# Kernel optimization log

Hardware: AMD Instinct MI355X
Metric: run time of the kernel (lower is better)

The kernel has to match this reference:

```python
import jax, jax.numpy as jnp
import numpy as np

EMB = 1024
HEADS = 16
HEAD_SZ = EMB // HEADS
EPS = 1e-5


def _layernorm(x, g, b):
    mu = jnp.mean(x, axis=-1, keepdims=True)
    var = jnp.mean(jnp.square(x - mu), axis=-1, keepdims=True)
    return (x - mu) * jax.lax.rsqrt(var + EPS) * g + b


def setup_inputs() -> dict:
    key = jax.random.key(0)
    ks = jax.random.split(key, 12)
    s_in = 1.0 / np.sqrt(EMB)
    s_h = 1.0 / np.sqrt(4 * EMB)
    return {
        "x": jax.random.normal(ks[0], (4, 1024, EMB), jnp.float32),
        # per-head Q/K/V projections stacked: [H, EMB, HEAD_SZ], no bias
        "wq": jax.random.normal(ks[1], (HEADS, EMB, HEAD_SZ), jnp.float32) * s_in,
        "wk": jax.random.normal(ks[2], (HEADS, EMB, HEAD_SZ), jnp.float32) * s_in,
        "wv": jax.random.normal(ks[3], (HEADS, EMB, HEAD_SZ), jnp.float32) * s_in,
        "w_proj": jax.random.normal(ks[4], (EMB, EMB), jnp.float32) * s_in,
        "b_proj": jnp.zeros((EMB,), jnp.float32),
        "w1": jax.random.normal(ks[5], (EMB, 4 * EMB), jnp.float32) * s_in,
        "b1": jnp.zeros((4 * EMB,), jnp.float32),
        "w2": jax.random.normal(ks[6], (4 * EMB, EMB), jnp.float32) * s_h,
        "b2": jnp.zeros((EMB,), jnp.float32),
        "g1": jnp.ones((EMB,), jnp.float32),
        "be1": jnp.zeros((EMB,), jnp.float32),
        "g2": jnp.ones((EMB,), jnp.float32),
        "be2": jnp.zeros((EMB,), jnp.float32),
    }


def reference(x, wq, wk, wv, w_proj, b_proj, w1, b1, w2, b2, g1, be1, g2, be2):
    B, T, C = x.shape
    # --- self-attention (pre-norm) ---
    h = _layernorm(x, g1, be1)
    q = jnp.einsum("btc,hcd->bhtd", h, wq)
    k = jnp.einsum("btc,hcd->bhtd", h, wk)
    v = jnp.einsum("btc,hcd->bhtd", h, wv)
    scale = 1.0 / jnp.sqrt(jnp.asarray(HEAD_SZ, x.dtype))
    scores = jnp.einsum("bhtd,bhsd->bhts", q, k) * scale  # non-causal: SDPA called with no mask
    attn = jax.nn.softmax(scores, axis=-1)
    o = jnp.einsum("bhts,bhsd->bhtd", attn, v)
    o = o.transpose(0, 2, 1, 3).reshape(B, T, C)  # concat heads (same order as torch.cat)
    sa_out = o @ w_proj + b_proj
    x = x + sa_out
    # --- feed-forward; note ln2 applied twice, faithful to source ---
    t = _layernorm(x, g2, be2)
    t = _layernorm(t, g2, be2)
    ff = jax.nn.relu(t @ w1 + b1) @ w2 + b2
    return x + ff
```

## Files before the change

### kernel.cpp

```cpp
#include <hip/hip_runtime.h>
#include <hip/hip_bf16.h>
#include <math.h>
#include <stdint.h>

typedef __bf16 bf16_t;
typedef __bf16 bf16x4 __attribute__((ext_vector_type(4)));
typedef __bf16 bf16x8 __attribute__((ext_vector_type(8)));
typedef float floatx4 __attribute__((ext_vector_type(4)));

#define BM 128
#define BK 32

__device__ __forceinline__ size_t ftaddr(int m, int k, int KT) {
    return ((size_t)(m >> 4) * KT + (k >> 5)) * 512
         + (((k >> 3) & 3) * 16 + (m & 15)) * 8 + (k & 7);
}

__device__ __forceinline__ void gload16(const void* g, void* lds) {
    __builtin_amdgcn_global_load_lds(
        (__attribute__((address_space(1))) void*)(uintptr_t)g,
        (__attribute__((address_space(3))) void*)(uintptr_t)lds,
        16, 0, 0);
}

template<int N>
__device__ __forceinline__ void waitvm_barrier() {
    if constexpr (N == 0)       asm volatile("s_waitcnt vmcnt(0)\n\ts_barrier" ::: "memory");
    else if constexpr (N == 4)  asm volatile("s_waitcnt vmcnt(4)\n\ts_barrier" ::: "memory");
    else if constexpr (N == 6)  asm volatile("s_waitcnt vmcnt(6)\n\ts_barrier" ::: "memory");
    else if constexpr (N == 8)  asm volatile("s_waitcnt vmcnt(8)\n\ts_barrier" ::: "memory");
    else if constexpr (N == 12) asm volatile("s_waitcnt vmcnt(12)\n\ts_barrier" ::: "memory");
    else if constexpr (N == 16) asm volatile("s_waitcnt vmcnt(16)\n\ts_barrier" ::: "memory");
    else static_assert(N == 0, "unsupported vmcnt");
}

__device__ __forceinline__ void waitvm_barrier_rt(int n) {
    switch (n) {
    case 12: asm volatile("s_waitcnt vmcnt(12)\n\ts_barrier" ::: "memory"); break;
    case 8:  asm volatile("s_waitcnt vmcnt(8)\n\ts_barrier"  ::: "memory"); break;
    case 6:  asm volatile("s_waitcnt vmcnt(6)\n\ts_barrier"  ::: "memory"); break;
    case 4:  asm volatile("s_waitcnt vmcnt(4)\n\ts_barrier"  ::: "memory"); break;
    default: asm volatile("s_waitcnt vmcnt(0)\n\ts_barrier"  ::: "memory"); break;
    }
}

__global__ void prep_kernel(const float* __restrict__ wq, const float* __restrict__ wk,
                            const float* __restrict__ wv, const float* __restrict__ w_proj,
                            const float* __restrict__ w1, const float* __restrict__ w2,
                            bf16_t* __restrict__ WQKVT, bf16_t* __restrict__ WPROJT,
                            bf16_t* __restrict__ W1T, bf16_t* __restrict__ W2T,
                            const float* __restrict__ x, const float* __restrict__ g1,
                            const float* __restrict__ be1, bf16_t* __restrict__ HB)
{
    __shared__ __align__(16) char psm[33024];
    const int tid = threadIdx.x;
    if (blockIdx.x < 3072) {
        float (*tile)[65] = (float(*)[65])psm;
        const int idx = blockIdx.x;
        const float* in; bf16_t* out; int R, C, rt, ct; long nrow0;
        if (idx < 768) {
            const int z = idx >> 8;
            const int hd = (idx >> 4) & 15;
            rt = idx & 15; ct = 0; R = 1024; C = 64;
            in  = (z == 0 ? wq : z == 1 ? wk : wv) + hd * 65536;
            out = WQKVT; nrow0 = z * 1024 + hd * 64;
        } else if (idx < 1024) {
            const int t = idx - 768; rt = t & 15; ct = t >> 4; R = 1024; C = 1024;
            in = w_proj; out = WPROJT; nrow0 = 0;
        } else if (idx < 2048) {
            const int t = idx - 1024; rt = t & 15; ct = t >> 4; R = 1024; C = 4096;
            in = w1; out = W1T; nrow0 = 0;
        } else {
            const int t = idx - 2048; rt = t & 63; ct = t >> 6; R = 4096; C = 1024;
            in = w2; out = W2T; nrow0 = 0;
        }
        const int r0 = rt * 64, c0 = ct * 64;
        const int tr = tid >> 4;
        const int tc = (tid & 15) * 4;
#pragma unroll
        for (int rr = 0; rr < 4; rr++) {
            const int r = tr + rr * 16;
            const float4 v = *(const float4*)&in[(long)(r0 + r) * C + c0 + tc];
            tile[r][tc + 0] = v.x; tile[r][tc + 1] = v.y;
            tile[r][tc + 2] = v.z; tile[r][tc + 3] = v.w;
        }
        __syncthreads();
        const int KT = R >> 5;
        const int w = tid >> 6, l = tid & 63;
        const int c = l >> 4, rr2 = l & 15;
#pragma unroll
        for (int it = 0; it < 2; ++it) {
            const int t8 = it * 4 + w;
            const int kt = t8 >> 2;
            const int nb = t8 & 3;
            const long n = nrow0 + c0 + nb * 16 + rr2;
            const int k = r0 + kt * 32 + c * 8;
            bf16x8 o;
#pragma unroll
            for (int e = 0; e < 8; e++)
                o[e] = (bf16_t)tile[kt * 32 + c * 8 + e][nb * 16 + rr2];
            *(bf16x8*)&out[ftaddr((int)n, k, KT)] = o;
        }
    } else {
        bf16_t (*ybuf)[1032] = (bf16_t(*)[1032])psm;
        const int wave = tid >> 6, lane = tid & 63;
        const int rb = blockIdx.x - 3072;
        float4 gvv[4], bvv[4];
#pragma unroll
        for (int j = 0; j < 4; j++) {
            gvv[j] = ((const float4*)g1)[lane + j * 64];
            bvv[j] = ((const float4*)be1)[lane + j * 64];
        }
#pragma unroll
        for (int rr = 0; rr < 4; ++rr) {
            const int lrow = wave * 4 + rr;
            const float* xr = x + (size_t)(rb * 16 + lrow) * 1024;
            float4 v[4];
            float s = 0.f, s2 = 0.f;
#pragma unroll
            for (int j = 0; j < 4; j++) {
                v[j] = ((const float4*)xr)[lane + j * 64];
                s  += v[j].x + v[j].y + v[j].z + v[j].w;
                s2 += v[j].x * v[j].x + v[j].y * v[j].y + v[j].z * v[j].z + v[j].w * v[j].w;
            }
#pragma unroll
            for (int off = 32; off >= 1; off >>= 1) {
                s  += __shfl_xor(s, off);
                s2 += __shfl_xor(s2, off);
            }
            const float mu = s * (1.0f / 1024.0f);
            const float rs = rsqrtf(fmaxf(s2 * (1.0f / 1024.0f) - mu * mu, 0.f) + 1e-5f);
#pragma unroll
            for (int j = 0; j < 4; j++) {
                bf16x4 o;
                o[0] = (bf16_t)((v[j].x - mu) * rs * gvv[j].x + bvv[j].x);
                o[1] = (bf16_t)((v[j].y - mu) * rs * gvv[j].y + bvv[j].y);
                o[2] = (bf16_t)((v[j].z - mu) * rs * gvv[j].z + bvv[j].z);
                o[3] = (bf16_t)((v[j].w - mu) * rs * gvv[j].w + bvv[j].w);
                *(bf16x4*)&ybuf[lrow][(lane + j * 64) * 4] = o;
            }
        }
        __syncthreads();
        bf16_t* outBase = HB + (size_t)rb * 32 * 512;
#pragma unroll
        for (int it = 0; it < 8; ++it) {
            const int s = it * 256 + tid;
            const int kt = s >> 6, c = (s >> 4) & 3, rr2 = s & 15;
            const bf16x8 val = *(const bf16x8*)&ybuf[rr2][kt * 32 + c * 8];
            *(bf16x8*)&outBase[(size_t)s * 8] = val;
        }
    }
}

__global__ void ln2x_kernel(const float* __restrict__ x, const float* __restrict__ g,
                            const float* __restrict__ b, bf16_t* __restrict__ outb)
{
    __shared__ __align__(16) bf16_t ybuf[16][1032];
    const int tid = threadIdx.x, wave = tid >> 6, lane = tid & 63;
    const int rb = blockIdx.x;
    float4 gvv[4], bvv[4];
#pragma unroll
    for (int j = 0; j < 4; j++) {
        gvv[j] = ((const float4*)g)[lane + j * 64];
        bvv[j] = ((const float4*)b)[lane + j * 64];
    }
#pragma unroll
    for (int rr = 0; rr < 4; ++rr) {
        const int lrow = wave * 4 + rr;
        const float* xr = x + (size_t)(rb * 16 + lrow) * 1024;
        float4 v[4];
        float s = 0.f, s2 = 0.f;
#pragma unroll
        for (int j = 0; j < 4; j++) {
            v[j] = ((const float4*)xr)[lane + j * 64];
            s  += v[j].x + v[j].y + v[j].z + v[j].w;
            s2 += v[j].x * v[j].x + v[j].y * v[j].y + v[j].z * v[j].z + v[j].w * v[j].w;
        }
#pragma unroll
        for (int off = 32; off >= 1; off >>= 1) {
            s  += __shfl_xor(s, off);
            s2 += __shfl_xor(s2, off);
        }
        float mu = s * (1.0f / 1024.0f);
        float rs = rsqrtf(fmaxf(s2 * (1.0f / 1024.0f) - mu * mu, 0.f) + 1e-5f);
        s = 0.f; s2 = 0.f;
#pragma unroll
        for (int j = 0; j < 4; j++) {
            v[j].x = (v[j].x - mu) * rs * gvv[j].x + bvv[j].x;
            v[j].y = (v[j].y - mu) * rs * gvv[j].y + bvv[j].y;
            v[j].z = (v[j].z - mu) * rs * gvv[j].z + bvv[j].z;
            v[j].w = (v[j].w - mu) * rs * gvv[j].w + bvv[j].w;
            s  += v[j].x + v[j].y + v[j].z + v[j].w;
            s2 += v[j].x * v[j].x + v[j].y * v[j].y + v[j].z * v[j].z + v[j].w * v[j].w;
        }
#pragma unroll
        for (int off = 32; off >= 1; off >>= 1) {
            s  += __shfl_xor(s, off);
            s2 += __shfl_xor(s2, off);
        }
        mu = s * (1.0f / 1024.0f);
        rs = rsqrtf(fmaxf(s2 * (1.0f / 1024.0f) - mu * mu, 0.f) + 1e-5f);
#pragma unroll
        for (int j = 0; j < 4; j++) {
            bf16x4 o;
            o[0] = (bf16_t)((v[j].x - mu) * rs * gvv[j].x + bvv[j].x);
            o[1] = (bf16_t)((v[j].y - mu) * rs * gvv[j].y + bvv[j].y);
            o[2] = (bf16_t)((v[j].z - mu) * rs * gvv[j].z + bvv[j].z);
            o[3] = (bf16_t)((v[j].w - mu) * rs * gvv[j].w + bvv[j].w);
            *(bf16x4*)&ybuf[lrow][(lane + j * 64) * 4] = o;
        }
    }
    __syncthreads();
    bf16_t* outBase = outb + (size_t)rb * 32 * 512;
#pragma unroll
    for (int it = 0; it < 8; ++it) {
        const int s = it * 256 + tid;
        const int kt = s >> 6, c = (s >> 4) & 3, rr2 = s & 15;
        const bf16x8 val = *(const bf16x8*)&ybuf[rr2][kt * 32 + c * 8];
        *(bf16x8*)&outBase[(size_t)s * 8] = val;
    }
}

template<int EPI, int BNt, int DEPTH>
__global__ __launch_bounds__(256, 2)
void gemm_bt(const bf16_t* __restrict__ A, const bf16_t* __restrict__ Bt,
             const int K,
             const float* __restrict__ bias, const float* __restrict__ resid,
             float* __restrict__ outf, bf16_t* __restrict__ outb,
             bf16_t* __restrict__ aux1, bf16_t* __restrict__ aux2,
             const int Nout)
{
    constexpr int NFRAG = 4;
    constexpr int AI    = (BNt == 128) ? 4 : 2;
    constexpr int LPS   = (BNt == 128) ? 4 : 3;
    constexpr int ASZ = DEPTH * 8 * 512;
    constexpr int BSZ = DEPTH * (BNt / 16) * 512;
    __shared__ __align__(16) bf16_t smem[ASZ + BSZ];
    bf16_t* Asb = smem;
    bf16_t* Bsb = smem + ASZ;
    const int tid  = threadIdx.x;
    const int wave = tid >> 6, lane = tid & 63;
    const int wr = wave >> 1, wc = wave & 1;
    const int bm = blockIdx.x * BM, bn = blockIdx.y * BNt;
    const int KT = K >> 5;

    floatx4 acc[AI][NFRAG];
#pragma unroll
    for (int i = 0; i < AI; i++)
#pragma unroll
        for (int j = 0; j < NFRAG; j++) acc[i][j] = (floatx4){0.f, 0.f, 0.f, 0.f};

    const bf16_t* gA0 = A + ((size_t)(bm / 16 + wave * 2 + 0) * KT) * 512 + lane * 8;
    const bf16_t* gA1 = A + ((size_t)(bm / 16 + wave * 2 + 1) * KT) * 512 + lane * 8;
    const int lA0 = (wave * 2 + 0) * 512;
    const int lA1 = (wave * 2 + 1) * 512;

    const bf16_t* gB0;
    const bf16_t* gB1 = nullptr;
    int lB0;
    if (BNt == 128) {
        gB0 = Bt + ((size_t)(bn / 16 + wave * 2 + 0) * KT) * 512 + lane * 8;
        gB1 = Bt + ((size_t)(bn / 16 + wave * 2 + 1) * KT) * 512 + lane * 8;
        lB0 = 0;
    } else {
        gB0 = Bt + ((size_t)(bn / 16 + wave) * KT) * 512 + lane * 8;
        lB0 = wave * 512;
    }

    auto stage = [&](int t, int bu) {
        const size_t off = (size_t)t * 512;
        gload16(gA0 + off, Asb + bu * 4096 + lA0);
        gload16(gA1 + off, Asb + bu * 4096 + lA1);
        if (BNt == 128) {
            gload16(gB0 + off, Bsb + bu * 4096 + lA0);
            gload16(gB1 + off, Bsb + bu * 4096 + lA1);
        } else {
            gload16(gB0 + off, Bsb + bu * (4 * 512) + lB0);
        }
    };

    auto compute = [&](int bu) {
        bf16x8 af[AI], bfv[NFRAG];
        if (BNt == 128) {
#pragma unroll
            for (int i = 0; i < AI; i++)
                af[i] = *(const bf16x8*)&Asb[bu * 4096 + (wr * 4 + i) * 512 + lane * 8];
#pragma unroll
            for (int j = 0; j < NFRAG; j++)
                bfv[j] = *(const bf16x8*)&Bsb[bu * 4096 + (wc * 4 + j) * 512 + lane * 8];
        } else {
#pragma unroll
            for (int i = 0; i < AI; i++)
                af[i] = *(const bf16x8*)&Asb[bu * 4096 + (wave * 2 + i) * 512 + lane * 8];
#pragma unroll
            for (int j = 0; j < NFRAG; j++)
                bfv[j] = *(const bf16x8*)&Bsb[bu * (4 * 512) + j * 512 + lane * 8];
        }
#pragma unroll
        for (int i = 0; i < AI; i++)
#pragma unroll
            for (int j = 0; j < NFRAG; j++)
                acc[i][j] = __builtin_amdgcn_mfma_f32_16x16x32_bf16(af[i], bfv[j], acc[i][j], 0, 0, 0);
    };

    const int NT = K / BK;
    if (BNt == 64) {
#pragma unroll
        for (int i = 0; i < DEPTH - 2; ++i) stage(i, i);
        int t = 0;
        for (; t + 5 < NT; t += 2) {
            waitvm_barrier<LPS * 2>();
            stage(t + 4, (t + 4) % DEPTH);
            compute(t % DEPTH);
            stage(t + 5, (t + 5) % DEPTH);
            compute((t + 1) % DEPTH);
        }
        waitvm_barrier<LPS * 2>();
        compute((NT - 4) % DEPTH);
        compute((NT - 3) % DEPTH);
        waitvm_barrier<0>();
        compute((NT - 2) % DEPTH);
        compute((NT - 1) % DEPTH);
    } else {
#pragma unroll
        for (int i = 0; i < DEPTH - 1; ++i) stage(i, i);
        int bu = 0;
        for (int t = 0; t <= NT - DEPTH; ++t) {
            waitvm_barrier<LPS * (DEPTH - 2)>();
            stage(t + DEPTH - 1, bu == 0 ? DEPTH - 1 : bu - 1);
            compute(bu);
            bu = (bu + 1 == DEPTH) ? 0 : bu + 1;
        }
#pragma unroll
        for (int j = DEPTH - 2; j >= 0; --j) {
            waitvm_barrier_rt(LPS * j);
            compute(bu);
            bu = (bu + 1 == DEPTH) ? 0 : bu + 1;
        }
    }

    const int er = (lane >> 4) * 4, ec = lane & 15;
    if constexpr (BNt == 128) {
        if (EPI == 0 && bn >= 2048) {
            __syncthreads();
            bf16_t* scr = smem;
#pragma unroll
            for (int i = 0; i < AI; i++)
#pragma unroll
                for (int j = 0; j < NFRAG; j++)
#pragma unroll
                    for (int r = 0; r < 4; r++)
                        scr[((wc * 4 + j) * 16 + ec) * 136 + (wr * 4 + i) * 16 + er + r] =
                            (bf16_t)acc[i][j][r];
            __syncthreads();
            const int bq = bm >> 10, tmod = bm & 1023, h0 = (bn - 2048) >> 6;
#pragma unroll
            for (int it = 0; it < 8; ++it) {
                const int c = it * 256 + tid;
                const int dl = c >> 4, t16 = c & 15;
                const bf16x8 val = *(const bf16x8*)&scr[dl * 136 + t16 * 8];
                const int h = h0 + (dl >> 6), dd = dl & 63;
                *(bf16x8*)&aux2[(size_t)((bq * 16 + h) * 64 + dd) * 1024 + tmod + t16 * 8] = val;
            }
            return;
        }
    }
#pragma unroll
    for (int i = 0; i < AI; i++) {
#pragma unroll
        for (int j = 0; j < NFRAG; j++) {
            const int col = (BNt == 128) ? (bn + (wc * 4 + j) * 16 + ec)
                                         : (bn + j * 16 + ec);
#pragma unroll
            for (int r = 0; r < 4; r++) {
                const int row = (BNt == 128) ? (bm + (wr * 4 + i) * 16 + er + r)
                                             : (bm + wave * 32 + i * 16 + er + r);
                const float v = acc[i][j][r];
                if (EPI == 0) {
                    const int b = row >> 10, t = row & 1023;
                    if (col < 1024) {
                        const int h = col >> 6, d = col & 63;
                        outb[(size_t)((b * 16 + h) * 1024 + t) * 64 + d] = (bf16_t)v;
                    } else {
                        const int c2 = col - 1024, h = c2 >> 6, d = c2 & 63;
                        aux1[(size_t)((b * 16 + h) * 1024 + t) * 64 + d] = (bf16_t)v;
                    }
                } else if (EPI == 1 || EPI == 3) {
                    const size_t idx = (size_t)row * Nout + col;
                    outf[idx] = v + bias[col] + resid[idx];
                } else if (EPI == 2) {
                    outb[ftaddr(row, col, Nout >> 5)] = (bf16_t)fmaxf(v + bias[col], 0.f);
                }
            }
        }
    }
}

__global__ __launch_bounds__(256, 4)
void attn_kernel(const bf16_t* __restrict__ Q, const bf16_t* __restrict__ Kg,
                 const bf16_t* __restrict__ Vt, bf16_t* __restrict__ Og)
{
    __shared__ __align__(16) bf16_t Ks[2][4096];
    __shared__ __align__(16) bf16_t Vs[2][4096];
    __shared__ __align__(16) bf16_t Ps[4][1024];
    const int tid = threadIdx.x, wave = tid >> 6, lane = tid & 63;
    const int lin = blockIdx.x + (blockIdx.y << 4);
    const int xcd = lin & 7, idx = lin >> 3;
    const int bh = xcd * 8 + (idx >> 4);
    const int qt = idx & 15;
    const int b = bh >> 4, h = bh & 15;
    const int q0 = qt * 64 + wave * 16;
    const bf16_t* Qb = Q + (size_t)bh * 65536;
    const char* Kb = (const char*)(Kg + (size_t)bh * 65536);
    const char* Vb = (const char*)(Vt + (size_t)bh * 65536);
    const int fr = lane & 15, g = lane >> 4, fk = g * 8;

    const bf16x8 qf0 = *(const bf16x8*)&Qb[(size_t)(q0 + fr) * 64 + fk];
    const bf16x8 qf1 = *(const bf16x8*)&Qb[(size_t)(q0 + fr) * 64 + 32 + fk];

    floatx4 o[4];
#pragma unroll
    for (int dt = 0; dt < 4; dt++) o[dt] = (floatx4){0.f, 0.f, 0.f, 0.f};
    float lsum[4] = {0.f, 0.f, 0.f, 0.f};
    bf16_t* pw = &Ps[wave][0];
    const float sscale = 0.125f * 1.44269504088896f;

    auto stage = [&](int s0, int bu) {
#pragma unroll
        for (int t = 0; t < 2; t++) {
            const int j = wave * 2 + t;
            gload16(Kb + (size_t)(s0 + lane) * 128 + j * 16, &Ks[bu][j * 512]);
            gload16(Vb + (size_t)lane * 2048 + (size_t)s0 * 2 + j * 16, &Vs[bu][j * 512]);
        }
    };

    stage(0, 0);
    int bu = 0;
    for (int it = 0; it < 16; ++it) {
        __syncthreads();
        if (it < 15) stage((it + 1) * 64, bu ^ 1);
        const bf16_t* Kl = Ks[bu];
        const bf16_t* Vl = Vs[bu];

        floatx4 sacc[4];
#pragma unroll
        for (int ss = 0; ss < 4; ss++) sacc[ss] = (floatx4){0.f, 0.f, 0.f, 0.f};
        __builtin_amdgcn_s_setprio(1);
#pragma unroll
        for (int ss = 0; ss < 4; ss++) {
#pragma unroll
            for (int c = 0; c < 2; c++) {
                const int ch = c * 4 + g;
                const bf16x8 qf = (c == 0) ? qf0 : qf1;
                const bf16x8 kf = *(const bf16x8*)&Kl[ch * 512 + (ss * 16 + fr) * 8];
                sacc[ss] = __builtin_amdgcn_mfma_f32_16x16x32_bf16(qf, kf, sacc[ss], 0, 0, 0);
            }
        }
        __builtin_amdgcn_s_setprio(0);
#pragma unroll
        for (int ss = 0; ss < 2; ss++) {
#pragma unroll
            for (int r = 0; r < 4; r++) {
                const float p = __builtin_amdgcn_exp2f(sacc[ss][r] * sscale);
                lsum[r] += p;
                const int q = g * 4 + r;
                pw[(ss * 2 + (fr >> 3)) * 128 + q * 8 + (fr & 7)] = (bf16_t)p;
            }
        }
        asm volatile("s_waitcnt lgkmcnt(0)" ::: "memory");
#pragma unroll
        for (int ss = 2; ss < 4; ss++) {
#pragma unroll
            for (int r = 0; r < 4; r++) {
                const float p = __builtin_amdgcn_exp2f(sacc[ss][r] * sscale);
                lsum[r] += p;
                const int q = g * 4 + r;
                pw[(ss * 2 + (fr >> 3)) * 128 + q * 8 + (fr & 7)] = (bf16_t)p;
            }
        }
        {
            const int ch = g;
            const bf16x8 pf = *(const bf16x8*)&pw[ch * 128 + fr * 8];
            __builtin_amdgcn_s_setprio(1);
#pragma unroll
            for (int dt = 0; dt < 4; dt++) {
                const bf16x8 vf = *(const bf16x8*)&Vl[ch * 512 + (dt * 16 + fr) * 8];
                o[dt] = __builtin_amdgcn_mfma_f32_16x16x32_bf16(pf, vf, o[dt], 0, 0, 0);
            }
            __builtin_amdgcn_s_setprio(0);
        }
        asm volatile("s_waitcnt lgkmcnt(0)" ::: "memory");
        {
            const int ch = 4 + g;
            const bf16x8 pf = *(const bf16x8*)&pw[ch * 128 + fr * 8];
            __builtin_amdgcn_s_setprio(1);
#pragma unroll
            for (int dt = 0; dt < 4; dt++) {
                const bf16x8 vf = *(const bf16x8*)&Vl[ch * 512 + (dt * 16 + fr) * 8];
                o[dt] = __builtin_amdgcn_mfma_f32_16x16x32_bf16(pf, vf, o[dt], 0, 0, 0);
            }
            __builtin_amdgcn_s_setprio(0);
        }
        asm volatile("" ::: "memory");
        bu ^= 1;
    }
#pragma unroll
    for (int r = 0; r < 4; r++) {
        float l = lsum[r];
        l += __shfl_xor(l, 1);
        l += __shfl_xor(l, 2);
        l += __shfl_xor(l, 4);
        l += __shfl_xor(l, 8);
        lsum[r] = 1.0f / l;
    }
    const int tq = q0 + g * 4;
#pragma unroll
    for (int dt = 0; dt < 4; dt++) {
#pragma unroll
        for (int r = 0; r < 4; r++) {
            const int m = b * 1024 + tq + r;
            const int k = h * 64 + dt * 16 + fr;
            Og[ftaddr(m, k, 32)] = (bf16_t)(o[dt][r] * lsum[r]);
        }
    }
}

extern "C" void kernel_launch(void* const* d_in, const int* in_sizes, int n_in,
                              void* d_out, int out_size, void* d_ws, size_t ws_size,
                              hipStream_t stream)
{
    const float* x      = (const float*)d_in[0];
    const float* wq     = (const float*)d_in[1];
    const float* wk     = (const float*)d_in[2];
    const float* wv     = (const float*)d_in[3];
    const float* w_proj = (const float*)d_in[4];
    const float* b_proj = (const float*)d_in[5];
    const float* w1     = (const float*)d_in[6];
    const float* b1     = (const float*)d_in[7];
    const float* w2     = (const float*)d_in[8];
    const float* b2     = (const float*)d_in[9];
    const float* g1     = (const float*)d_in[10];
    const float* be1    = (const float*)d_in[11];
    const float* g2     = (const float*)d_in[12];
    const float* be2    = (const float*)d_in[13];
    float* out = (float*)d_out;
    char* ws = (char*)d_ws;

    bf16_t* WQKVT = (bf16_t*)(ws + 0x0000000);
    bf16_t* WPROJT= (bf16_t*)(ws + 0x0600000);
    bf16_t* W1T   = (bf16_t*)(ws + 0x0800000);
    bf16_t* W2T   = (bf16_t*)(ws + 0x1000000);
    bf16_t* HB    = (bf16_t*)(ws + 0x1800000);
    bf16_t* Qb    = (bf16_t*)(ws + 0x2000000);
    bf16_t* Kb    = (bf16_t*)(ws + 0x2800000);
    bf16_t* Vtb   = (bf16_t*)(ws + 0x3000000);
    bf16_t* AO    = (bf16_t*)(ws + 0x3800000);
    float*  X2    = (float*)(ws + 0x4000000);
    bf16_t* TB    = (bf16_t*)(ws + 0x2800000);
    bf16_t* FF1B  = (bf16_t*)(ws + 0x5000000);

    dim3 blk(256);
    prep_kernel<<<3328, blk, 0, stream>>>(wq, wk, wv, w_proj, w1, w2,
                                          WQKVT, WPROJT, W1T, W2T,
                                          x, g1, be1, HB);
    gemm_bt<0, 128, 5><<<dim3(32, 24), blk, 0, stream>>>(HB, WQKVT, 1024, nullptr, nullptr,
                                                         nullptr, Qb, Kb, Vtb, 3072);
    attn_kernel<<<dim3(16, 64), blk, 0, stream>>>(Qb, Kb, Vtb, AO);
    gemm_bt<1, 64, 6><<<dim3(32, 16), blk, 0, stream>>>(AO, WPROJT, 1024, b_proj, x,
                                                        X2, nullptr, nullptr, nullptr, 1024);
    ln2x_kernel<<<256, blk, 0, stream>>>(X2, g2, be2, TB);
    gemm_bt<2, 128, 5><<<dim3(32, 32), blk, 0, stream>>>(TB, W1T, 1024, b1, nullptr,
                                                         nullptr, FF1B, nullptr, nullptr, 4096);
    gemm_bt<3, 64, 6><<<dim3(32, 16), blk, 0, stream>>>(FF1B, W2T, 4096, b2, X2,
                                                        out, nullptr, nullptr, nullptr, 1024);
}
```

Baseline: 307.2 us.

## Split-K the FF2 GEMM with BN=128 tiles and add XCD-aware block remap

The final FF2 GEMM (K=4096) now uses 128-wide N tiles split across two K halves via gridDim.z, writing fp32 partials that a new reduce kernel sums with bias and residual. All GEMMs also get an XCD-aware block index remap so neighbouring tiles share an XCD's L2. This aims to raise per-block reuse and keep enough blocks in flight for the long-K GEMM. The cost is an extra 32MB of partial-sum writes and reads plus one more kernel launch.

New measurement: 328.9 us. 1.07x slower.

```diff
diff --git a/kernel.cpp b/kernel.cpp
--- a/kernel.cpp
+++ b/kernel.cpp
@@ -221,6 +221,28 @@
     }
 }
 
+__global__ void reduce2_kernel(const float* __restrict__ p,
+                               const float* __restrict__ bias,
+                               const float* __restrict__ resid,
+                               float* __restrict__ out)
+{
+    const int base = blockIdx.x * 256 + threadIdx.x;
+#pragma unroll
+    for (int it = 0; it < 2; ++it) {
+        const int i = base + it * 524288;
+        const float4 a = ((const float4*)p)[i];
+        const float4 b = ((const float4*)p)[i + 1048576];
+        const float4 r = ((const float4*)resid)[i];
+        const float4 bs = ((const float4*)bias)[i & 255];
+        float4 o;
+        o.x = a.x + b.x + r.x + bs.x;
+        o.y = a.y + b.y + r.y + bs.y;
+        o.z = a.z + b.z + r.z + bs.z;
+        o.w = a.w + b.w + r.w + bs.w;
+        ((float4*)out)[i] = o;
+    }
+}
+
 template<int EPI, int BNt, int DEPTH>
 __global__ __launch_bounds__(256, 2)
 void gemm_bt(const bf16_t* __restrict__ A, const bf16_t* __restrict__ Bt,
@@ -228,7 +250,7 @@
              const float* __restrict__ bias, const float* __restrict__ resid,
              float* __restrict__ outf, bf16_t* __restrict__ outb,
              bf16_t* __restrict__ aux1, bf16_t* __restrict__ aux2,
-             const int Nout)
+             const int Nout, const int ntloc)
 {
     constexpr int NFRAG = 4;
     constexpr int AI    = (BNt == 128) ? 4 : 2;
@@ -241,8 +263,14 @@
     const int tid  = threadIdx.x;
     const int wave = tid >> 6, lane = tid & 63;
     const int wr = wave >> 1, wc = wave & 1;
-    const int bm = blockIdx.x * BM, bn = blockIdx.y * BNt;
+
+    const int lin = blockIdx.x + (blockIdx.y << 5);
+    const int xcd = lin & 7, idx = lin >> 3;
+    const int nbx = idx & 31;
+    const int nby = xcd * (gridDim.y >> 3) + (idx >> 5);
+    const int bm = nbx * BM, bn = nby * BNt;
     const int KT = K >> 5;
+    const int kb0 = blockIdx.z * ntloc;
 
     floatx4 acc[AI][NFRAG];
 #pragma unroll
@@ -250,8 +278,8 @@
 #pragma unroll
         for (int j = 0; j < NFRAG; j++) acc[i][j] = (floatx4){0.f, 0.f, 0.f, 0.f};
 
-    const bf16_t* gA0 = A + ((size_t)(bm / 16 + wave * 2 + 0) * KT) * 512 + lane * 8;
-    const bf16_t* gA1 = A + ((size_t)(bm / 16 + wave * 2 + 1) * KT) * 512 + lane * 8;
+    const bf16_t* gA0 = A + ((size_t)(bm / 16 + wave * 2 + 0) * KT + kb0) * 512 + lane * 8;
+    const bf16_t* gA1 = A + ((size_t)(bm / 16 + wave * 2 + 1) * KT + kb0) * 512 + lane * 8;
     const int lA0 = (wave * 2 + 0) * 512;
     const int lA1 = (wave * 2 + 1) * 512;
 
@@ -259,11 +287,11 @@
     const bf16_t* gB1 = nullptr;
     int lB0;
     if (BNt == 128) {
-        gB0 = Bt + ((size_t)(bn / 16 + wave * 2 + 0) * KT) * 512 + lane * 8;
-        gB1 = Bt + ((size_t)(bn / 16 + wave * 2 + 1) * KT) * 512 + lane * 8;
+        gB0 = Bt + ((size_t)(bn / 16 + wave * 2 + 0) * KT + kb0) * 512 + lane * 8;
+        gB1 = Bt + ((size_t)(bn / 16 + wave * 2 + 1) * KT + kb0) * 512 + lane * 8;
         lB0 = 0;
     } else {
-        gB0 = Bt + ((size_t)(bn / 16 + wave) * KT) * 512 + lane * 8;
+        gB0 = Bt + ((size_t)(bn / 16 + wave) * KT + kb0) * 512 + lane * 8;
         lB0 = wave * 512;
     }
 
@@ -303,7 +331,7 @@
                 acc[i][j] = __builtin_amdgcn_mfma_f32_16x16x32_bf16(af[i], bfv[j], acc[i][j], 0, 0, 0);
     };
 
-    const int NT = K / BK;
+    const int NT = ntloc;
     if (BNt == 64) {
 #pragma unroll
         for (int i = 0; i < DEPTH - 2; ++i) stage(i, i);
@@ -390,6 +418,8 @@
                     outf[idx] = v + bias[col] + resid[idx];
                 } else if (EPI == 2) {
                     outb[ftaddr(row, col, Nout >> 5)] = (bf16_t)fmaxf(v + bias[col], 0.f);
+                } else if (EPI == 4) {
+                    outf[(size_t)blockIdx.z * (4096u * 1024u) + (size_t)row * Nout + col] = v;
                 }
             }
         }
@@ -558,19 +588,21 @@
     float*  X2    = (float*)(ws + 0x4000000);
     bf16_t* TB    = (bf16_t*)(ws + 0x2800000);
     bf16_t* FF1B  = (bf16_t*)(ws + 0x5000000);
+    float*  P2    = (float*)(ws + 0x1800000);
 
     dim3 blk(256);
     prep_kernel<<<3328, blk, 0, stream>>>(wq, wk, wv, w_proj, w1, w2,
                                           WQKVT, WPROJT, W1T, W2T,
                                           x, g1, be1, HB);
     gemm_bt<0, 128, 5><<<dim3(32, 24), blk, 0, stream>>>(HB, WQKVT, 1024, nullptr, nullptr,
-                                                         nullptr, Qb, Kb, Vtb, 3072);
+                                                         nullptr, Qb, Kb, Vtb, 3072, 32);
     attn_kernel<<<dim3(16, 64), blk, 0, stream>>>(Qb, Kb, Vtb, AO);
     gemm_bt<1, 64, 6><<<dim3(32, 16), blk, 0, stream>>>(AO, WPROJT, 1024, b_proj, x,
-                                                        X2, nullptr, nullptr, nullptr, 1024);
+                                                        X2, nullptr, nullptr, nullptr, 1024, 32);
     ln2x_kernel<<<256, blk, 0, stream>>>(X2, g2, be2, TB);
     gemm_bt<2, 128, 5><<<dim3(32, 32), blk, 0, stream>>>(TB, W1T, 1024, b1, nullptr,
-                                                         nullptr, FF1B, nullptr, nullptr, 4096);
-    gemm_bt<3, 64, 6><<<dim3(32, 16), blk, 0, stream>>>(FF1B, W2T, 4096, b2, X2,
-                                                        out, nullptr, nullptr, nullptr, 1024);
-}
+                                                         nullptr, FF1B, nullptr, nullptr, 4096, 32);
+    gemm_bt<4, 128, 5><<<dim3(32, 8, 2), blk, 0, stream>>>(FF1B, W2T, 4096, nullptr, nullptr,
+                                                           P2, nullptr, nullptr, nullptr, 1024, 64);
+    reduce2_kernel<<<2048, blk, 0, stream>>>(P2, b2, X2, out);
+}
```
